# Performance work log

Measured on AMD Instinct MI355X. Metric: run time of the kernel, lower is better.

The kernel has to match this reference:

```python
import jax, jax.numpy as jnp
import numpy as np

N = 50000      # nodes
E = 1600000    # edges (nnz of A)
D_IN = 512
D_H = 512
D_OUT = 40
L = 3
LN_EPS = 1e-5
BN_EPS = 1e-5


def setup_inputs() -> dict:
    key = jax.random.key(0)
    ks = jax.random.split(key, 10)
    x = jax.random.normal(ks[0], (N, D_IN), dtype=jnp.float32)
    edge_src = jax.random.randint(ks[1], (E,), 0, N, dtype=jnp.int32)
    edge_dst = jax.random.randint(ks[2], (E,), 0, N, dtype=jnp.int32)
    s = 1.0 / np.sqrt(D_IN)
    W_in = (jax.random.normal(ks[3], (D_IN, D_H), dtype=jnp.float32) * s)
    b_in = jnp.zeros((D_H,), jnp.float32)
    ln_g = jnp.ones((D_H,), jnp.float32)
    ln_b = jnp.zeros((D_H,), jnp.float32)
    cW1 = (jax.random.normal(ks[4], (D_H, D_H), dtype=jnp.float32) * s)
    cb1 = jnp.zeros((D_H,), jnp.float32)
    bn_g = 1.0 + 0.1 * jax.random.normal(ks[5], (D_H,), dtype=jnp.float32)
    bn_b = 0.1 * jax.random.normal(ks[6], (D_H,), dtype=jnp.float32)
    bn_mean = jnp.zeros((D_H,), jnp.float32)   # eval-mode running stats
    bn_var = jnp.ones((D_H,), jnp.float32)
    cW2 = (jax.random.normal(ks[7], (D_H, D_OUT), dtype=jnp.float32) * s)
    cb2 = jnp.zeros((D_OUT,), jnp.float32)
    return dict(x=x, edge_src=edge_src, edge_dst=edge_dst, W_in=W_in, b_in=b_in,
                ln_g=ln_g, ln_b=ln_b, cW1=cW1, cb1=cb1, bn_g=bn_g, bn_b=bn_b,
                bn_mean=bn_mean, bn_var=bn_var, cW2=cW2, cb2=cb2)


def _agg_angle(h, edge_src, edge_dst, dinv):
    # diag(D^-1/2 A D^-1/2 @ CosSim^T)[i] = sum_{(i,j) in A} dinv_i dinv_j cos(h_i,h_j)
    nrm = jnp.sqrt(jnp.sum(h * h, axis=1, keepdims=True))  # torch.norm p=2
    hn = h / (nrm + 1e-4)
    cos_e = jnp.clip(jnp.sum(hn[edge_src] * hn[edge_dst], axis=1), -1.0, 1.0)  # [E]
    w_e = dinv[edge_src] * dinv[edge_dst] * cos_e
    return jax.ops.segment_sum(w_e, edge_src, num_segments=N)  # [N]


def _forward(x, edge_src, edge_dst, W_in, b_in, ln_g, ln_b, cW1, cb1,
             bn_g, bn_b, bn_mean, bn_var, cW2, cb2):
    h = jax.nn.relu(x @ W_in + b_in)
    mu = jnp.mean(h, axis=-1, keepdims=True)
    var = jnp.var(h, axis=-1, keepdims=True)
    h = (h - mu) / jnp.sqrt(var + LN_EPS) * ln_g + ln_b   # LayerNorm
    # dropout: eval mode -> identity
    # degree normalization (adjacency values are all 1.0); constant across layers
    deg = jax.ops.segment_sum(jnp.ones((E,), h.dtype), edge_src, num_segments=N)
    dinv = jnp.where(deg > 0, deg ** -0.5, 0.0)
    for _ in range(L):
        ang = _agg_angle(h, edge_src, edge_dst, dinv)  # [N]
        c, s = jnp.cos(ang), jnp.sin(ang)
        r0 = c * h[:, 0] - s * h[:, 1]   # 2x2 Givens rotation on first two dims
        r1 = s * h[:, 0] + c * h[:, 1]
        h = jnp.concatenate([jnp.stack([r0, r1], axis=1), h[:, 2:]], axis=1)
    # classifier: Linear -> ReLU -> BatchNorm1d (eval) -> Linear
    z = jax.nn.relu(h @ cW1 + cb1)
    z = (z - bn_mean) / jnp.sqrt(bn_var + BN_EPS) * bn_g + bn_b
    logits = z @ cW2 + cb2
    return jax.nn.log_softmax(logits, axis=1)


def reference(x, edge_src, edge_dst, W_in, b_in, ln_g, ln_b, cW1, cb1,
              bn_g, bn_b, bn_mean, bn_var, cW2, cb2):
    return _forward(x, edge_src, edge_dst, W_in, b_in, ln_g, ln_b, cW1, cb1,
                    bn_g, bn_b, bn_mean, bn_var, cW2, cb2)
```

## Files before the change

### kernel.cpp

```cpp
#include <hip/hip_runtime.h>
#include <hip/hip_bf16.h>
#include <math.h>

typedef unsigned short u16;
typedef unsigned int u32;

#define N_NODES 50000
#define N_EDGES 1600000
#define DIM     512
#define DOUT    40
#define MPAD    50048
#define QROW    256
#define NBKT    196
#define NB1     256
#define CHUNK   6250

typedef __bf16 bf16x8 __attribute__((ext_vector_type(8)));
typedef float  f32x4  __attribute__((ext_vector_type(4)));

__device__ inline u16 f2bf(float f) {
    union { float f; u32 u; } v; v.f = f;
    u32 u = v.u;
    u32 r = u + 0x7fffu + ((u >> 16) & 1u);
    return (u16)(r >> 16);
}
__device__ inline float2 bfpair(u32 u) {
    float2 r;
    union { u32 i; float f; } lo, hi;
    lo.i = u << 16; hi.i = u & 0xffff0000u;
    r.x = lo.f; r.y = hi.f; return r;
}
__device__ inline float wave_sum(float v) {
    #pragma unroll
    for (int o = 32; o > 0; o >>= 1) v += __shfl_xor(v, o);
    return v;
}
__device__ inline float wave_max(float v) {
    #pragma unroll
    for (int o = 32; o > 0; o >>= 1) v = fmaxf(v, __shfl_xor(v, o));
    return v;
}
__device__ inline int wave_sum_i(int v) {
    #pragma unroll
    for (int o = 32; o > 0; o >>= 1) v += __shfl_xor(v, o);
    return v;
}
#if __has_builtin(__builtin_amdgcn_sdot8)
__device__ inline int dot8(int a, int b, int c) {
    return __builtin_amdgcn_sdot8(a, b, c, false);
}
#else
__device__ inline int dot8(int a, int b, int c) {
    #pragma unroll
    for (int j = 0; j < 8; ++j) {
        int av = ((int)((u32)a << (28 - 4 * j))) >> 28;
        int bv = ((int)((u32)b << (28 - 4 * j))) >> 28;
        c += av * bv;
    }
    return c;
}
#endif
__device__ inline void gload16(const void* g, void* l) {
    __builtin_amdgcn_global_load_lds((const __attribute__((address_space(1))) u32*)g,
                                     (__attribute__((address_space(3))) u32*)l, 16, 0, 0);
}
__device__ inline int block_incl_scan(int v, int tid) {
    int lane = tid & 63, w = tid >> 6;
    #pragma unroll
    for (int o = 1; o < 64; o <<= 1) {
        int t = __shfl_up(v, o);
        if (lane >= o) v += t;
    }
    __shared__ int wsum[4];
    if (lane == 63) wsum[w] = v;
    __syncthreads();
    if (w > 0) v += wsum[0];
    if (w > 1) v += wsum[1];
    if (w > 2) v += wsum[2];
    return v;
}

__global__ __launch_bounds__(256) void k_conv_x(const float* __restrict__ x,
                                                u16* __restrict__ xb) {
    long idx = (long)blockIdx.x * 256 + threadIdx.x;
    long base = idx * 4;
    if (base >= (long)MPAD * DIM) return;
    long row = base >> 9;
    float4 v;
    if (row < N_NODES) v = *(const float4*)(x + base);
    else { v.x = v.y = v.z = v.w = 0.f; }
    ushort4 o;
    o.x = f2bf(v.x); o.y = f2bf(v.y); o.z = f2bf(v.z); o.w = f2bf(v.w);
    *(ushort4*)(xb + base) = o;
}

__global__ __launch_bounds__(256) void k_prep(const float* __restrict__ W_in,
                                              const float* __restrict__ cW1,
                                              const float* __restrict__ cW2,
                                              u16* __restrict__ WtIn,
                                              u16* __restrict__ W1t,
                                              u16* __restrict__ W2b) {
    int z = blockIdx.z;
    if (z < 2) {
        const float* W = z ? cW1 : W_in;
        u16* T = z ? W1t : WtIn;
        int n = blockIdx.x * 16 + threadIdx.x;
        int k = blockIdx.y * 16 + threadIdx.y;
        T[(long)n * 512 + k] = f2bf(W[(long)k * 512 + n]);
    } else {
        int idx = (blockIdx.y * 32 + blockIdx.x) * 256 + threadIdx.y * 16 + threadIdx.x;
        if (idx < 48 * DIM) {
            int n = idx >> 9;
            int k = idx & 511;
            float v = (n < DOUT) ? cW2[(long)k * DOUT + n] : 0.f;
            W2b[idx] = f2bf(v);
        }
    }
}

__global__ __launch_bounds__(256) void k_ms_count(const int* __restrict__ esrc,
                                                  int* __restrict__ C) {
    __shared__ int bcnt[NBKT];
    int tid = threadIdx.x, blk = blockIdx.x;
    if (tid < NBKT) bcnt[tid] = 0;
    __syncthreads();
    int e0 = blk * CHUNK, e1 = e0 + CHUNK;
    for (int e = e0 + tid; e < e1; e += 256)
        atomicAdd(&bcnt[esrc[e] >> 8], 1);
    __syncthreads();
    if (tid < NBKT) C[tid * NB1 + blk] = bcnt[tid];
}
__global__ __launch_bounds__(256) void k_ms_scan_partial(const int* __restrict__ C,
                                                         int* __restrict__ psum2) {
    int v = C[blockIdx.x * 256 + threadIdx.x];
    int t = wave_sum_i(v);
    __shared__ int ws[4];
    int lane = threadIdx.x & 63, w = threadIdx.x >> 6;
    if (lane == 0) ws[w] = t;
    __syncthreads();
    if (threadIdx.x == 0) psum2[blockIdx.x] = ws[0] + ws[1] + ws[2] + ws[3];
}
__global__ __launch_bounds__(256) void k_ms_scan_base(const int* __restrict__ psum2,
                                                      int* __restrict__ pb2) {
    int tid = threadIdx.x;
    int v = (tid < NBKT) ? psum2[tid] : 0;
    int incl = block_incl_scan(v, tid);
    if (tid < NBKT) pb2[tid] = incl - v;
}
__global__ __launch_bounds__(256) void k_ms_scan_add(const int* __restrict__ C,
                                                     const int* __restrict__ pb2,
                                                     int* __restrict__ O) {
    int idx = blockIdx.x * 256 + threadIdx.x;
    int v = C[idx];
    int incl = block_incl_scan(v, threadIdx.x);
    O[idx] = pb2[blockIdx.x] + incl - v;
}
__global__ __launch_bounds__(256) void k_ms_scatter(const int* __restrict__ esrc,
                                                    const int* __restrict__ edst,
                                                    const int* __restrict__ O,
                                                    u32* __restrict__ pk) {
    __shared__ int cur[NBKT];
    int tid = threadIdx.x, blk = blockIdx.x;
    if (tid < NBKT) cur[tid] = O[tid * NB1 + blk];
    __syncthreads();
    int e0 = blk * CHUNK, e1 = e0 + CHUNK;
    for (int e = e0 + tid; e < e1; e += 256) {
        int s = esrc[e], d = edst[e];
        int pos = atomicAdd(&cur[s >> 8], 1);
        pk[pos] = ((u32)(s & 255) << 16) | (u32)d;
    }
}
__global__ __launch_bounds__(256) void k_bucket(const int* __restrict__ Om,
                                                const u32* __restrict__ pk,
                                                int* __restrict__ rowptr,
                                                float* __restrict__ dinv,
                                                int* __restrict__ edst_s) {
    __shared__ int cnt[256];
    __shared__ int curs[256];
    int tid = threadIdx.x, b = blockIdx.x;
    int base = b * 256;
    int start = Om[b * NB1];
    int end = (b == NBKT - 1) ? N_EDGES : Om[(b + 1) * NB1];
    cnt[tid] = 0;
    __syncthreads();
    for (int p = start + tid; p < end; p += 256)
        atomicAdd(&cnt[pk[p] >> 16], 1);
    __syncthreads();
    int c = cnt[tid];
    int incl = block_incl_scan(c, tid);
    int excl = incl - c;
    int node = base + tid;
    if (node < N_NODES) {
        rowptr[node] = start + excl;
        dinv[node] = (c > 0) ? (1.f / sqrtf((float)c)) : 0.f;
    }
    if (b == NBKT - 1 && tid == 0) rowptr[N_NODES] = N_EDGES;
    curs[tid] = start + excl;
    __syncthreads();
    for (int p = start + tid; p < end; p += 256) {
        u32 pr = pk[p];
        int pos = atomicAdd(&curs[pr >> 16], 1);
        edst_s[pos] = (int)(pr & 0xFFFFu);
    }
}

template<int EPI>
__global__ __launch_bounds__(256) void k_gemm(const u16* __restrict__ A,
                                              const u16* __restrict__ Bt,
                                              u16* __restrict__ outB,
                                              const float* __restrict__ bias,
                                              const float* __restrict__ bn_g,
                                              const float* __restrict__ bn_b,
                                              const float* __restrict__ bn_mean,
                                              const float* __restrict__ bn_var) {
    __shared__ u16 lds[2 * 128 * 64];
    char* ldsA = (char*)lds;
    char* ldsB = (char*)lds + 16384;

    const int bid = blockIdx.x;
    const int xcd = bid & 7;
    const int j = bid >> 3;
    const int tm = xcd * 49 + (j >> 2);
    const int tn = j & 3;
    if (tm >= MPAD / 128) return;

    const int tid = threadIdx.x;
    const int l = tid & 63, wid = tid >> 6;
    const int wr = wid >> 1, wc = wid & 1;
    const int lm = l & 15, lk = l >> 4;

    const int srow = tid >> 3;
    const int kq   = tid & 7;

    f32x4 acc[4][4] = {};

    for (int kt = 0; kt < 8; ++kt) {
        const int k0 = kt * 64;
        #pragma unroll
        for (int r = 0; r < 4; ++r) {
            int row = r * 32 + srow;
            int kc = (kq ^ (row & 7)) * 8;
            const u16* ga = A + ((long)tm * 128 + row) * DIM + k0 + kc;
            const u16* gb = Bt + ((long)tn * 128 + row) * DIM + k0 + kc;
            char* la = ldsA + r * 4096 + wid * 1024;
            char* lb = ldsB + r * 4096 + wid * 1024;
            gload16(ga, la);
            gload16(gb, lb);
        }
        __syncthreads();
        #pragma unroll
        for (int kk = 0; kk < 2; ++kk) {
            bf16x8 af[4], bfr[4];
            #pragma unroll
            for (int m = 0; m < 4; ++m) {
                int ar = wr * 64 + m * 16 + lm;
                af[m] = *(const bf16x8*)(ldsA + ar * 128 + ((kk * 64 + lk * 16) ^ ((ar & 7) << 4)));
            }
            #pragma unroll
            for (int n = 0; n < 4; ++n) {
                int br = wc * 64 + n * 16 + lm;
                bfr[n] = *(const bf16x8*)(ldsB + br * 128 + ((kk * 64 + lk * 16) ^ ((br & 7) << 4)));
            }
            #pragma unroll
            for (int m = 0; m < 4; ++m)
                #pragma unroll
                for (int n = 0; n < 4; ++n)
                    acc[m][n] = __builtin_amdgcn_mfma_f32_16x16x32_bf16(af[m], bfr[n], acc[m][n], 0, 0, 0);
        }
        __syncthreads();
    }

    #pragma unroll
    for (int n = 0; n < 4; ++n) {
        int col = tn * 128 + wc * 64 + n * 16 + lm;
        float bc = bias[col];
        float scale = 0.f, shift = 0.f;
        if (EPI == 1) {
            scale = bn_g[col] / sqrtf(bn_var[col] + 1e-5f);
            shift = bn_b[col] - bn_mean[col] * scale;
        }
        #pragma unroll
        for (int m = 0; m < 4; ++m) {
            f32x4 v = acc[m][n];
            #pragma unroll
            for (int r = 0; r < 4; ++r) {
                long row = (long)tm * 128 + wr * 64 + m * 16 + lk * 4 + r;
                float val = fmaxf(v[r] + bc, 0.f);
                if (EPI == 1) val = val * scale + shift;
                outB[row * DIM + col] = f2bf(val);
            }
        }
    }
}

__global__ __launch_bounds__(256) void k_ln(u16* __restrict__ hb,
                                            char* __restrict__ hq,
                                            float* __restrict__ stepr,
                                            const float* __restrict__ g,
                                            const float* __restrict__ b,
                                            float* __restrict__ a0,
                                            float* __restrict__ a1,
                                            float* __restrict__ inv_nrm) {
    int row = blockIdx.x * 4 + (threadIdx.x >> 6);
    int l = threadIdx.x & 63;
    u16* prow = hb + (long)row * DIM + l * 8;
    if (row >= N_NODES) {
        if (row < MPAD) { uint4 z; z.x = z.y = z.z = z.w = 0u; *(uint4*)prow = z; }
        return;
    }
    uint4 v = *(const uint4*)prow;
    float x[8];
    { float2 p;
      p = bfpair(v.x); x[0] = p.x; x[1] = p.y;
      p = bfpair(v.y); x[2] = p.x; x[3] = p.y;
      p = bfpair(v.z); x[4] = p.x; x[5] = p.y;
      p = bfpair(v.w); x[6] = p.x; x[7] = p.y; }
    float s = 0.f, sq = 0.f;
    #pragma unroll
    for (int j = 0; j < 8; ++j) { s += x[j]; sq += x[j] * x[j]; }
    #pragma unroll
    for (int o = 32; o > 0; o >>= 1) { s += __shfl_xor(s, o); sq += __shfl_xor(sq, o); }
    float mean = s * (1.f / DIM);
    float var = sq * (1.f / DIM) - mean * mean;
    float rstd = 1.f / sqrtf(var + 1e-5f);
    float y[8];
    #pragma unroll
    for (int j = 0; j < 8; ++j) {
        int c = l * 8 + j;
        y[j] = (x[j] - mean) * rstd * g[c] + b[c];
    }
    float s2 = 0.f;
    #pragma unroll
    for (int j = 0; j < 8; ++j) s2 += y[j] * y[j];
    s2 = wave_sum(s2);
    float nrm = sqrtf(s2);
    float inv = 1.f / (nrm + 1e-4f);
    ushort4 oh;
    oh.x = f2bf(y[0]); oh.y = f2bf(y[1]); oh.z = f2bf(y[2]); oh.w = f2bf(y[3]);
    *(ushort4*)prow = oh;
    oh.x = f2bf(y[4]); oh.y = f2bf(y[5]); oh.z = f2bf(y[6]); oh.w = f2bf(y[7]);
    *(ushort4*)(prow + 4) = oh;
    float nv[8];
    float mx = 0.f;
    #pragma unroll
    for (int j = 0; j < 8; ++j) { nv[j] = y[j] * inv; mx = fmaxf(mx, fabsf(nv[j])); }
    mx = wave_max(mx);
    float qs = (mx > 0.f) ? (7.f / mx) : 0.f;
    if (l == 0) { nv[0] = 0.f; nv[1] = 0.f; }
    u32 w = 0;
    #pragma unroll
    for (int j = 0; j < 8; ++j) {
        int q = (int)rintf(nv[j] * qs);
        w |= ((u32)(q & 0xF)) << (4 * j);
    }
    *(u32*)(hq + (long)row * QROW + l * 4) = w;
    if (l == 0) {
        stepr[row] = (mx > 0.f) ? (mx * (1.f / 7.f)) : 0.f;
        a0[row] = y[0]; a1[row] = y[1]; inv_nrm[row] = inv;
    }
}

__global__ __launch_bounds__(256) void k_edge_dot(const int* __restrict__ rowptr,
                                                  const int* __restrict__ edst_s,
                                                  const char* __restrict__ hq,
                                                  const float* __restrict__ stepr,
                                                  const float* __restrict__ a0i,
                                                  const float* __restrict__ a1i,
                                                  const float* __restrict__ invn,
                                                  const float* __restrict__ dinv,
                                                  float* __restrict__ rest,
                                                  float* __restrict__ a0o,
                                                  float* __restrict__ a1o) {
    int node = blockIdx.x * 4 + (threadIdx.x >> 6);
    if (node >= N_NODES) return;
    int l = threadIdx.x & 63;
    int le = l & 7;
    int eg = l >> 3;
    int p0 = rowptr[node], p1 = rowptr[node + 1];
    float xa = a0i[node], ya = a1i[node];
    if (p0 == p1) {
        if (l == 0) { a0o[node] = xa; a1o[node] = ya; }
        return;
    }
    const int4* srow = (const int4*)(hq + (long)node * QROW);
    int4 s0 = srow[le * 2], s1 = srow[le * 2 + 1];
    float ss = stepr[node];
    float si = invn[node];
    float sa0 = xa * si, sa1 = ya * si;
    float accum = 0.f;
    #pragma unroll 4
    for (int base = p0; base < p1; base += 8) {
        int p = base + eg;
        bool ok = p < p1;
        int d = ok ? edst_s[p] : 0;
        const int4* drow = (const int4*)(hq + (long)d * QROW);
        int4 d0 = drow[le * 2], d1 = drow[le * 2 + 1];
        int acc = 0;
        acc = dot8(s0.x, d0.x, acc); acc = dot8(s0.y, d0.y, acc);
        acc = dot8(s0.z, d0.z, acc); acc = dot8(s0.w, d0.w, acc);
        acc = dot8(s1.x, d1.x, acc); acc = dot8(s1.y, d1.y, acc);
        acc = dot8(s1.z, d1.z, acc); acc = dot8(s1.w, d1.w, acc);
        acc += __shfl_xor(acc, 4);
        acc += __shfl_xor(acc, 2);
        acc += __shfl_xor(acc, 1);
        if (ok && le == 0) {
            float r = ss * stepr[d] * (float)acc;
            rest[p] = r;
            float c = r + (sa0 * a0i[d] + sa1 * a1i[d]) * invn[d];
            c = fminf(1.f, fmaxf(-1.f, c));
            accum += dinv[d] * c;
        }
    }
    accum = wave_sum(accum);
    if (l == 0) {
        float ang = dinv[node] * accum;
        float sn, cs;
        sincosf(ang, &sn, &cs);
        a0o[node] = cs * xa - sn * ya;
        a1o[node] = sn * xa + cs * ya;
    }
}

template<int WRITE_HB>
__global__ __launch_bounds__(256) void k_layer(const int* __restrict__ rowptr,
                                               const int* __restrict__ edst_s,
                                               const float* __restrict__ rest,
                                               const float* __restrict__ a0i,
                                               const float* __restrict__ a1i,
                                               const float* __restrict__ invn,
                                               const float* __restrict__ dinv,
                                               float* __restrict__ a0o,
                                               float* __restrict__ a1o,
                                               u16* __restrict__ hb) {
    int node = blockIdx.x * 4 + (threadIdx.x >> 6);
    if (node >= N_NODES) return;
    int l = threadIdx.x & 63;
    int p0 = rowptr[node], p1 = rowptr[node + 1];
    float x = a0i[node], y = a1i[node];
    float si = invn[node];
    float sa0 = x * si, sa1 = y * si;
    float accum = 0.f;
    for (int p = p0 + l; p < p1; p += 64) {
        int d = edst_s[p];
        float c = rest[p] + (sa0 * a0i[d] + sa1 * a1i[d]) * invn[d];
        c = fminf(1.f, fmaxf(-1.f, c));
        accum += dinv[d] * c;
    }
    accum = wave_sum(accum);
    if (l == 0) {
        float ang = dinv[node] * accum;
        float sn, cs;
        sincosf(ang, &sn, &cs);
        float r0 = cs * x - sn * y;
        float r1 = sn * x + cs * y;
        a0o[node] = r0;
        a1o[node] = r1;
        if (WRITE_HB) {
            hb[(long)node * DIM + 0] = f2bf(r0);
            hb[(long)node * DIM + 1] = f2bf(r1);
        }
    }
}

__global__ __launch_bounds__(256) void k_final(const u16* __restrict__ zb,
                                               const u16* __restrict__ W2b,
                                               const float* __restrict__ cb2,
                                               float* __restrict__ out) {
    __shared__ char ldsB[48 * 1024];
    const int tid = threadIdx.x;
    #pragma unroll
    for (int i = 0; i < 12; ++i) {
        int unit = i * 256 + tid;
        int byte = unit * 16;
        int row = byte >> 10;
        int colb = byte & 1023;
        uint4 v = *(const uint4*)((const char*)W2b + byte);
        *(uint4*)(ldsB + row * 1024 + (colb ^ ((row & 7) << 4))) = v;
    }
    __syncthreads();

    const int l = tid & 63, wid = tid >> 6;
    const int lm = l & 15, lk = l >> 4;
    const long m0 = (long)blockIdx.x * 128 + wid * 32;

    f32x4 acc[2][3] = {};
    for (int kt = 0; kt < 16; ++kt) {
        const int k0 = kt * 32;
        bf16x8 af[2], bfr[3];
        #pragma unroll
        for (int m = 0; m < 2; ++m)
            af[m] = *(const bf16x8*)(zb + (m0 + m * 16 + lm) * DIM + k0 + lk * 8);
        #pragma unroll
        for (int n = 0; n < 3; ++n) {
            int br = n * 16 + lm;
            bfr[n] = *(const bf16x8*)(ldsB + br * 1024 + ((k0 * 2 + lk * 16) ^ ((br & 7) << 4)));
        }
        #pragma unroll
        for (int m = 0; m < 2; ++m)
            #pragma unroll
            for (int n = 0; n < 3; ++n)
                acc[m][n] = __builtin_amdgcn_mfma_f32_16x16x32_bf16(af[m], bfr[n], acc[m][n], 0, 0, 0);
    }

    float bc[3];
    #pragma unroll
    for (int n = 0; n < 3; ++n) {
        int col = n * 16 + lm;
        bc[n] = (col < DOUT) ? cb2[col] : 0.f;
    }

    #pragma unroll
    for (int m = 0; m < 2; ++m) {
        #pragma unroll
        for (int r = 0; r < 4; ++r) {
            long row = m0 + m * 16 + lk * 4 + r;
            float v[3];
            float mv = -1e30f;
            #pragma unroll
            for (int n = 0; n < 3; ++n) {
                int col = n * 16 + lm;
                float t = (col < DOUT) ? (acc[m][n][r] + bc[n]) : -1e30f;
                v[n] = t;
                mv = fmaxf(mv, t);
            }
            #pragma unroll
            for (int o = 8; o > 0; o >>= 1) mv = fmaxf(mv, __shfl_xor(mv, o));
            float es = 0.f;
            #pragma unroll
            for (int n = 0; n < 3; ++n) {
                int col = n * 16 + lm;
                if (col < DOUT) es += expf(v[n] - mv);
            }
            #pragma unroll
            for (int o = 8; o > 0; o >>= 1) es += __shfl_xor(es, o);
            float lse = logf(es);
            if (row < N_NODES) {
                #pragma unroll
                for (int n = 0; n < 3; ++n) {
                    int col = n * 16 + lm;
                    if (col < DOUT) out[row * DOUT + col] = v[n] - mv - lse;
                }
            }
        }
    }
}

extern "C" void kernel_launch(void* const* d_in, const int* in_sizes, int n_in,
                              void* d_out, int out_size, void* d_ws, size_t ws_size,
                              hipStream_t stream) {
    const float* x       = (const float*)d_in[0];
    const int*   esrc    = (const int*)d_in[1];
    const int*   edst    = (const int*)d_in[2];
    const float* W_in    = (const float*)d_in[3];
    const float* b_in    = (const float*)d_in[4];
    const float* ln_g    = (const float*)d_in[5];
    const float* ln_b    = (const float*)d_in[6];
    const float* cW1     = (const float*)d_in[7];
    const float* cb1     = (const float*)d_in[8];
    const float* bn_g    = (const float*)d_in[9];
    const float* bn_b    = (const float*)d_in[10];
    const float* bn_mean = (const float*)d_in[11];
    const float* bn_var  = (const float*)d_in[12];
    const float* cW2     = (const float*)d_in[13];
    const float* cb2     = (const float*)d_in[14];
    float* out = (float*)d_out;

    char* ws = (char*)d_ws;
    size_t off = 0;
    auto take = [&](size_t bytes) -> char* {
        char* p = ws + off;
        off = (off + bytes + 255) & ~(size_t)255;
        return p;
    };
    u16*   xb     = (u16*)take((size_t)MPAD * DIM * 2);
    u16*   hb     = (u16*)take((size_t)MPAD * DIM * 2);
    char*  hq     = (char*)take((size_t)N_NODES * QROW);
    float* stepr  = (float*)take((size_t)N_NODES * 4);
    u16*   WtIn   = (u16*)take((size_t)512 * 512 * 2);
    u16*   W1t    = (u16*)take((size_t)512 * 512 * 2);
    u16*   W2b    = (u16*)take((size_t)48 * 512 * 2);
    float* dinv   = (float*)take((size_t)N_NODES * 4);
    float* a0A    = (float*)take((size_t)N_NODES * 4);
    float* a1A    = (float*)take((size_t)N_NODES * 4);
    float* a0B    = (float*)take((size_t)N_NODES * 4);
    float* a1B    = (float*)take((size_t)N_NODES * 4);
    float* invn   = (float*)take((size_t)N_NODES * 4);
    float* rest   = (float*)take((size_t)N_EDGES * 4);
    int*   rowptr = (int*)take((size_t)(N_NODES + 1) * 4);
    int*   edst_s = (int*)take((size_t)N_EDGES * 4);
    u32*   pk     = (u32*)take((size_t)N_EDGES * 4);
    int*   Cm     = (int*)take((size_t)NBKT * NB1 * 4);
    int*   Om     = (int*)take((size_t)NBKT * NB1 * 4);
    int*   psum2  = (int*)take((size_t)NBKT * 4);
    int*   pb2    = (int*)take((size_t)NBKT * 4);
    u16*   zb     = xb;

    k_conv_x<<<(MPAD * DIM / 4 + 255) / 256, 256, 0, stream>>>(x, xb);
    k_prep<<<dim3(32, 32, 3), dim3(16, 16), 0, stream>>>(W_in, cW1, cW2, WtIn, W1t, W2b);

    k_ms_count<<<NB1, 256, 0, stream>>>(esrc, Cm);
    k_ms_scan_partial<<<NBKT, 256, 0, stream>>>(Cm, psum2);
    k_ms_scan_base<<<1, 256, 0, stream>>>(psum2, pb2);
    k_ms_scan_add<<<NBKT, 256, 0, stream>>>(Cm, pb2, Om);
    k_ms_scatter<<<NB1, 256, 0, stream>>>(esrc, edst, Om, pk);
    k_bucket<<<NBKT, 256, 0, stream>>>(Om, pk, rowptr, dinv, edst_s);

    k_gemm<0><<<1568, 256, 0, stream>>>(xb, WtIn, hb, b_in,
                                        nullptr, nullptr, nullptr, nullptr);
    k_ln<<<MPAD / 4, 256, 0, stream>>>(hb, hq, stepr, ln_g, ln_b, a0A, a1A, invn);
    k_edge_dot<<<(N_NODES + 3) / 4, 256, 0, stream>>>(rowptr, edst_s, hq, stepr,
                                                      a0A, a1A, invn, dinv, rest, a0B, a1B);
    k_layer<0><<<(N_NODES + 3) / 4, 256, 0, stream>>>(rowptr, edst_s, rest,
                                                      a0B, a1B, invn, dinv, a0A, a1A, nullptr);
    k_layer<1><<<(N_NODES + 3) / 4, 256, 0, stream>>>(rowptr, edst_s, rest,
                                                      a0A, a1A, invn, dinv, a0B, a1B, hb);

    k_gemm<1><<<1568, 256, 0, stream>>>(hb, W1t, zb, cb1,
                                        bn_g, bn_b, bn_mean, bn_var);
    k_final<<<MPAD / 128, 256, 0, stream>>>(zb, W2b, cb2, out);
}
```

Measured before the change: 343.0 us.

## Pack per-node gather data into float4 and shrink edge indices to u16

Per-node values read by neighbour gathers (normalized first two coords, dinv, quantization step) are packed into one float4 array, so each edge does one 16-byte gather instead of four or five scattered 4-byte loads. Edge destination indices are stored as 16-bit values to halve index traffic. Each layer now writes an updated float4 per node, which adds some stores, and the u16 index only holds because node ids fit in 16 bits as packed.

```diff
diff --git a/kernel.cpp b/kernel.cpp
--- a/kernel.cpp
+++ b/kernel.cpp
@@ -174,7 +174,7 @@
                                                 const u32* __restrict__ pk,
                                                 int* __restrict__ rowptr,
                                                 float* __restrict__ dinv,
-                                                int* __restrict__ edst_s) {
+                                                u16* __restrict__ edst_s) {
     __shared__ int cnt[256];
     __shared__ int curs[256];
     int tid = threadIdx.x, b = blockIdx.x;
@@ -200,7 +200,7 @@
     for (int p = start + tid; p < end; p += 256) {
         u32 pr = pk[p];
         int pos = atomicAdd(&curs[pr >> 16], 1);
-        edst_s[pos] = (int)(pr & 0xFFFFu);
+        edst_s[pos] = (u16)(pr & 0xFFFFu);
     }
 }
 
@@ -295,12 +295,13 @@
 
 __global__ __launch_bounds__(256) void k_ln(u16* __restrict__ hb,
                                             char* __restrict__ hq,
-                                            float* __restrict__ stepr,
+                                            const float* __restrict__ dinv,
                                             const float* __restrict__ g,
                                             const float* __restrict__ b,
                                             float* __restrict__ a0,
                                             float* __restrict__ a1,
-                                            float* __restrict__ inv_nrm) {
+                                            float* __restrict__ inv_nrm,
+                                            float4* __restrict__ nd) {
     int row = blockIdx.x * 4 + (threadIdx.x >> 6);
     int l = threadIdx.x & 63;
     u16* prow = hb + (long)row * DIM + l * 8;
@@ -355,44 +356,46 @@
     }
     *(u32*)(hq + (long)row * QROW + l * 4) = w;
     if (l == 0) {
-        stepr[row] = (mx > 0.f) ? (mx * (1.f / 7.f)) : 0.f;
+        float st = (mx > 0.f) ? (mx * (1.f / 7.f)) : 0.f;
         a0[row] = y[0]; a1[row] = y[1]; inv_nrm[row] = inv;
+        float4 n4; n4.x = y[0] * inv; n4.y = y[1] * inv; n4.z = dinv[row]; n4.w = st;
+        nd[row] = n4;
     }
 }
 
 __global__ __launch_bounds__(256) void k_edge_dot(const int* __restrict__ rowptr,
-                                                  const int* __restrict__ edst_s,
+                                                  const u16* __restrict__ edst_s,
                                                   const char* __restrict__ hq,
-                                                  const float* __restrict__ stepr,
+                                                  const float4* __restrict__ ndI,
                                                   const float* __restrict__ a0i,
                                                   const float* __restrict__ a1i,
                                                   const float* __restrict__ invn,
-                                                  const float* __restrict__ dinv,
                                                   float* __restrict__ rest,
                                                   float* __restrict__ a0o,
-                                                  float* __restrict__ a1o) {
+                                                  float* __restrict__ a1o,
+                                                  float4* __restrict__ ndO) {
     int node = blockIdx.x * 4 + (threadIdx.x >> 6);
     if (node >= N_NODES) return;
     int l = threadIdx.x & 63;
     int le = l & 7;
     int eg = l >> 3;
     int p0 = rowptr[node], p1 = rowptr[node + 1];
+    float4 own = ndI[node];
     float xa = a0i[node], ya = a1i[node];
     if (p0 == p1) {
-        if (l == 0) { a0o[node] = xa; a1o[node] = ya; }
+        if (l == 0) { a0o[node] = xa; a1o[node] = ya; ndO[node] = own; }
         return;
     }
     const int4* srow = (const int4*)(hq + (long)node * QROW);
     int4 s0 = srow[le * 2], s1 = srow[le * 2 + 1];
-    float ss = stepr[node];
-    float si = invn[node];
-    float sa0 = xa * si, sa1 = ya * si;
+    float ss = own.w;
+    float sa0 = own.x, sa1 = own.y;
     float accum = 0.f;
     #pragma unroll 4
     for (int base = p0; base < p1; base += 8) {
         int p = base + eg;
         bool ok = p < p1;
-        int d = ok ? edst_s[p] : 0;
+        int d = ok ? (int)edst_s[p] : 0;
         const int4* drow = (const int4*)(hq + (long)d * QROW);
         int4 d0 = drow[le * 2], d1 = drow[le * 2 + 1];
         int acc = 0;
@@ -404,60 +407,72 @@
         acc += __shfl_xor(acc, 2);
         acc += __shfl_xor(acc, 1);
         if (ok && le == 0) {
-            float r = ss * stepr[d] * (float)acc;
+            float4 ndd = ndI[d];
+            float r = ss * ndd.w * (float)acc;
             rest[p] = r;
-            float c = r + (sa0 * a0i[d] + sa1 * a1i[d]) * invn[d];
+            float c = r + sa0 * ndd.x + sa1 * ndd.y;
             c = fminf(1.f, fmaxf(-1.f, c));
-            accum += dinv[d] * c;
+            accum += ndd.z * c;
         }
     }
     accum = wave_sum(accum);
     if (l == 0) {
-        float ang = dinv[node] * accum;
+        float ang = own.z * accum;
         float sn, cs;
         sincosf(ang, &sn, &cs);
-        a0o[node] = cs * xa - sn * ya;
-        a1o[node] = sn * xa + cs * ya;
+        float r0 = cs * xa - sn * ya;
+        float r1 = sn * xa + cs * ya;
+        a0o[node] = r0;
+        a1o[node] = r1;
+        float inv = invn[node];
+        float4 n4; n4.x = r0 * inv; n4.y = r1 * inv; n4.z = own.z; n4.w = own.w;
+        ndO[node] = n4;
     }
 }
 
 template<int WRITE_HB>
 __global__ __launch_bounds__(256) void k_layer(const int* __restrict__ rowptr,
-                                               const int* __restrict__ edst_s,
+                                               const u16* __restrict__ edst_s,
                                                const float* __restrict__ rest,
+                                               const float4* __restrict__ ndI,
                                                const float* __restrict__ a0i,
                                                const float* __restrict__ a1i,
                                                const float* __restrict__ invn,
-                                               const float* __restrict__ dinv,
                                                float* __restrict__ a0o,
                                                float* __restrict__ a1o,
+                                               float4* __restrict__ ndO,
                                                u16* __restrict__ hb) {
     int node = blockIdx.x * 4 + (threadIdx.x >> 6);
     if (node >= N_NODES) return;
     int l = threadIdx.x & 63;
     int p0 = rowptr[node], p1 = rowptr[node + 1];
+    float4 own = ndI[node];
     float x = a0i[node], y = a1i[node];
-    float si = invn[node];
-    float sa0 = x * si, sa1 = y * si;
+    float sa0 = own.x, sa1 = own.y;
     float accum = 0.f;
     for (int p = p0 + l; p < p1; p += 64) {
-        int d = edst_s[p];
-        float c = rest[p] + (sa0 * a0i[d] + sa1 * a1i[d]) * invn[d];
+        int d = (int)edst_s[p];
+        float4 ndd = ndI[d];
+        float c = rest[p] + sa0 * ndd.x + sa1 * ndd.y;
         c = fminf(1.f, fmaxf(-1.f, c));
-        accum += dinv[d] * c;
+        accum += ndd.z * c;
     }
     accum = wave_sum(accum);
     if (l == 0) {
-        float ang = dinv[node] * accum;
+        float ang = own.z * accum;
         float sn, cs;
         sincosf(ang, &sn, &cs);
         float r0 = cs * x - sn * y;
         float r1 = sn * x + cs * y;
-        a0o[node] = r0;
-        a1o[node] = r1;
         if (WRITE_HB) {
             hb[(long)node * DIM + 0] = f2bf(r0);
             hb[(long)node * DIM + 1] = f2bf(r1);
+        } else {
+            a0o[node] = r0;
+            a1o[node] = r1;
+            float inv = invn[node];
+            float4 n4; n4.x = r0 * inv; n4.y = r1 * inv; n4.z = own.z; n4.w = own.w;
+            ndO[node] = n4;
         }
     }
 }
@@ -572,28 +587,29 @@
         off = (off + bytes + 255) & ~(size_t)255;
         return p;
     };
-    u16*   xb     = (u16*)take((size_t)MPAD * DIM * 2);
-    u16*   hb     = (u16*)take((size_t)MPAD * DIM * 2);
-    char*  hq     = (char*)take((size_t)N_NODES * QROW);
-    float* stepr  = (float*)take((size_t)N_NODES * 4);
-    u16*   WtIn   = (u16*)take((size_t)512 * 512 * 2);
-    u16*   W1t    = (u16*)take((size_t)512 * 512 * 2);
-    u16*   W2b    = (u16*)take((size_t)48 * 512 * 2);
-    float* dinv   = (float*)take((size_t)N_NODES * 4);
-    float* a0A    = (float*)take((size_t)N_NODES * 4);
-    float* a1A    = (float*)take((size_t)N_NODES * 4);
-    float* a0B    = (float*)take((size_t)N_NODES * 4);
-    float* a1B    = (float*)take((size_t)N_NODES * 4);
-    float* invn   = (float*)take((size_t)N_NODES * 4);
-    float* rest   = (float*)take((size_t)N_EDGES * 4);
-    int*   rowptr = (int*)take((size_t)(N_NODES + 1) * 4);
-    int*   edst_s = (int*)take((size_t)N_EDGES * 4);
-    u32*   pk     = (u32*)take((size_t)N_EDGES * 4);
-    int*   Cm     = (int*)take((size_t)NBKT * NB1 * 4);
-    int*   Om     = (int*)take((size_t)NBKT * NB1 * 4);
-    int*   psum2  = (int*)take((size_t)NBKT * 4);
-    int*   pb2    = (int*)take((size_t)NBKT * 4);
-    u16*   zb     = xb;
+    u16*    xb     = (u16*)take((size_t)MPAD * DIM * 2);
+    u16*    hb     = (u16*)take((size_t)MPAD * DIM * 2);
+    char*   hq     = (char*)take((size_t)N_NODES * QROW);
+    u16*    WtIn   = (u16*)take((size_t)512 * 512 * 2);
+    u16*    W1t    = (u16*)take((size_t)512 * 512 * 2);
+    u16*    W2b    = (u16*)take((size_t)48 * 512 * 2);
+    float*  dinv   = (float*)take((size_t)N_NODES * 4);
+    float*  a0A    = (float*)take((size_t)N_NODES * 4);
+    float*  a1A    = (float*)take((size_t)N_NODES * 4);
+    float*  a0B    = (float*)take((size_t)N_NODES * 4);
+    float*  a1B    = (float*)take((size_t)N_NODES * 4);
+    float*  invn   = (float*)take((size_t)N_NODES * 4);
+    float4* ndA    = (float4*)take((size_t)N_NODES * 16);
+    float4* ndB    = (float4*)take((size_t)N_NODES * 16);
+    float*  rest   = (float*)take((size_t)N_EDGES * 4);
+    int*    rowptr = (int*)take((size_t)(N_NODES + 1) * 4);
+    u16*    edst_s = (u16*)take((size_t)N_EDGES * 2);
+    u32*    pk     = (u32*)take((size_t)N_EDGES * 4);
+    int*    Cm     = (int*)take((size_t)NBKT * NB1 * 4);
+    int*    Om     = (int*)take((size_t)NBKT * NB1 * 4);
+    int*    psum2  = (int*)take((size_t)NBKT * 4);
+    int*    pb2    = (int*)take((size_t)NBKT * 4);
+    u16*    zb     = xb;
 
     k_conv_x<<<(MPAD * DIM / 4 + 255) / 256, 256, 0, stream>>>(x, xb);
     k_prep<<<dim3(32, 32, 3), dim3(16, 16), 0, stream>>>(W_in, cW1, cW2, WtIn, W1t, W2b);
@@ -607,13 +623,13 @@
 
     k_gemm<0><<<1568, 256, 0, stream>>>(xb, WtIn, hb, b_in,
                                         nullptr, nullptr, nullptr, nullptr);
-    k_ln<<<MPAD / 4, 256, 0, stream>>>(hb, hq, stepr, ln_g, ln_b, a0A, a1A, invn);
-    k_edge_dot<<<(N_NODES + 3) / 4, 256, 0, stream>>>(rowptr, edst_s, hq, stepr,
-                                                      a0A, a1A, invn, dinv, rest, a0B, a1B);
-    k_layer<0><<<(N_NODES + 3) / 4, 256, 0, stream>>>(rowptr, edst_s, rest,
-                                                      a0B, a1B, invn, dinv, a0A, a1A, nullptr);
-    k_layer<1><<<(N_NODES + 3) / 4, 256, 0, stream>>>(rowptr, edst_s, rest,
-                                                      a0A, a1A, invn, dinv, a0B, a1B, hb);
+    k_ln<<<MPAD / 4, 256, 0, stream>>>(hb, hq, dinv, ln_g, ln_b, a0A, a1A, invn, ndA);
+    k_edge_dot<<<(N_NODES + 3) / 4, 256, 0, stream>>>(rowptr, edst_s, hq, ndA,
+                                                      a0A, a1A, invn, rest, a0B, a1B, ndB);
+    k_layer<0><<<(N_NODES + 3) / 4, 256, 0, stream>>>(rowptr, edst_s, rest, ndB,
+                                                      a0B, a1B, invn, a0A, a1A, ndA, nullptr);
+    k_layer<1><<<(N_NODES + 3) / 4, 256, 0, stream>>>(rowptr, edst_s, rest, ndA,
+                                                      a0A, a1A, invn, nullptr, nullptr, nullptr, hb);
 
     k_gemm<1><<<1568, 256, 0, stream>>>(hb, W1t, zb, cb1,
                                         bn_g, bn_b, bn_mean, bn_var);
```

After: 307.7 us. 10.3% less time.
